# Kernel tuning notes

Hardware: AMD Instinct MI355X
Metric: run time of the kernel (lower is better)

## Reference

```python
import jax, jax.numpy as jnp
import numpy as np

EPS = 1e-10
TEMP = 1.0


def setup_inputs() -> dict:
    key = jax.random.key(0)
    ks = jax.random.split(key, 8)
    num_nodes, embed_dim, hidden_dim, num_edges = 50000, 128, 64, 600000
    node_embed = jax.random.normal(ks[0], (num_nodes, embed_dim), dtype=jnp.float32)
    edge_index = jax.random.randint(ks[1], (2, num_edges), 0, num_nodes, dtype=jnp.int64)
    u1 = jax.random.uniform(ks[2], (num_edges,), dtype=jnp.float32)
    u2 = jax.random.uniform(ks[3], (num_edges,), dtype=jnp.float32)
    # Linear weights (kaiming-ish scale)
    W1 = jax.random.normal(ks[4], (2 * embed_dim, hidden_dim), dtype=jnp.float32) * (1.0 / np.sqrt(2 * embed_dim))
    b1 = jnp.zeros((hidden_dim,), dtype=jnp.float32)
    W2 = jax.random.normal(ks[5], (hidden_dim, 1), dtype=jnp.float32) * (1.0 / np.sqrt(hidden_dim))
    b2 = jnp.zeros((1,), dtype=jnp.float32)
    return {"node_embed": node_embed, "edge_index": edge_index, "u1": u1, "u2": u2,
            "W1": W1, "b1": b1, "W2": W2, "b2": b2}


def reference(node_embed, edge_index, u1, u2, W1, b1, W2, b2):
    row, col = edge_index[0], edge_index[1]
    # gather + concat: [num_edges, 2*embed_dim]
    edge_feat = jnp.concatenate([node_embed[row], node_embed[col]], axis=1)
    # small MLP (dropout is identity in eval)
    h = jax.nn.relu(edge_feat @ W1 + b1)
    edge_logits = (h @ W2 + b2).squeeze(-1)  # [num_edges]
    # Gumbel-sigmoid (soft)
    g1 = -jnp.log(-jnp.log(jnp.clip(u1, EPS, 1.0 - EPS)))
    g2 = -jnp.log(-jnp.log(jnp.clip(u2, EPS, 1.0 - EPS)))
    edge_probs = jax.nn.sigmoid((edge_logits + g1 - g2) / TEMP)
    return edge_probs
```

## Files before the change

### kernel.cpp

```cpp
#include <hip/hip_runtime.h>
#include <stdint.h>

typedef float  floatx4 __attribute__((ext_vector_type(4)));
typedef short  short8  __attribute__((ext_vector_type(8)));
typedef float  f4v     __attribute__((ext_vector_type(4)));
typedef unsigned int uint32;

#define GS_EPS 1e-10f

__device__ __forceinline__ unsigned short f2bf(float x) {
  uint32 u = __float_as_uint(x);
  u += 0x7FFFu + ((u >> 16) & 1u);
  return (unsigned short)(u >> 16);
}

__device__ __forceinline__ float i8tof(uint32 w, int j) {
  int b = (int)(w << (24 - 8 * j)) >> 24;
  return (float)b;
}

__device__ __forceinline__ uint32 pack4_i8(floatx4 a, float inv) {
  uint32 r = 0;
#pragma unroll
  for (int i = 0; i < 4; ++i) {
    float x = a[i] * inv;
    x = fminf(fmaxf(x, -127.f), 127.f);
    int v = (int)__builtin_rintf(x);
    r |= ((uint32)(v & 255)) << (8 * i);
  }
  return r;
}

__global__ void conv_w1cat_kernel(const float* __restrict__ W1,
                                  unsigned short* __restrict__ w1g) {
  int i = blockIdx.x * 256 + threadIdx.x;
  int chunk = i >> 7;
  int n = i & 127;
  const float* src = (n < 64) ? (W1 + n) : (W1 + 128 * 64 + (n - 64));
  uint32 d[4];
#pragma unroll
  for (int j = 0; j < 4; ++j) {
    int k0 = chunk * 8 + 2 * j;
    unsigned short lo = f2bf(src[(size_t)k0 * 64]);
    unsigned short hi = f2bf(src[(size_t)(k0 + 1) * 64]);
    d[j] = (uint32)lo | ((uint32)hi << 16);
  }
#pragma unroll
  for (int j = 0; j < 4; ++j) *(uint32*)&w1g[(size_t)i * 8 + 2 * j] = d[j];
}

__global__ __launch_bounds__(512, 4) void pcompute_kernel(
    const float* __restrict__ E, const unsigned short* __restrict__ w1g,
    const float* __restrict__ b1,
    uint8_t* __restrict__ P8top, uint8_t* __restrict__ P8bot,
    float* __restrict__ Sct, float* __restrict__ Scb, int num_nodes) {
  __shared__ __align__(16) unsigned short w1blk[16 * 128 * 8];

  const int tid = threadIdx.x;
  const int wave = tid >> 6;
  const int lane = tid & 63;
  const int q = lane >> 4;
  const int l16 = lane & 15;

#pragma unroll
  for (int it = 0; it < 4; ++it) {
    int idx = it * 512 + tid;
    short8 v = *(const short8*)(w1g + (size_t)idx * 8);
    *(short8*)&w1blk[(size_t)idx * 8] = v;
  }

  const int rowbase = blockIdx.x * 128 + wave * 16;
  int row = rowbase + l16;
  const bool ok = row < num_nodes;
  if (!ok) row = num_nodes - 1;

  short8 bfr[4];
#pragma unroll
  for (int kk = 0; kk < 4; ++kk) {
    const float* p = E + (size_t)row * 128 + kk * 32 + q * 8;
    f4v v0 = *(const f4v*)p;
    f4v v1 = *(const f4v*)(p + 4);
    short8 t;
    t[0] = (short)f2bf(v0[0]); t[1] = (short)f2bf(v0[1]);
    t[2] = (short)f2bf(v0[2]); t[3] = (short)f2bf(v0[3]);
    t[4] = (short)f2bf(v1[0]); t[5] = (short)f2bf(v1[1]);
    t[6] = (short)f2bf(v1[2]); t[7] = (short)f2bf(v1[3]);
    bfr[kk] = t;
  }
  __syncthreads();

  floatx4 acc[8];
#pragma unroll
  for (int t = 0; t < 8; ++t) {
    floatx4 z = {0.f, 0.f, 0.f, 0.f};
    acc[t] = z;
  }
#pragma unroll
  for (int kk = 0; kk < 4; ++kk) {
#pragma unroll
    for (int t = 0; t < 8; ++t) {
      short8 af = *(const short8*)&w1blk[(size_t)((kk * 4 + q) * 128 + t * 16 + l16) * 8];
      acc[t] = __builtin_amdgcn_mfma_f32_16x16x32_bf16(af, bfr[kk], acc[t], 0, 0, 0);
    }
  }

  float mtop = 0.f, mbot = 0.f;
#pragma unroll
  for (int t = 0; t < 8; ++t) {
    floatx4 a = acc[t];
    if (t < 4) {
      f4v bv = *(const f4v*)(b1 + t * 16 + q * 4);
      a[0] += bv[0]; a[1] += bv[1]; a[2] += bv[2]; a[3] += bv[3];
      acc[t] = a;
      mtop = fmaxf(mtop, fmaxf(fmaxf(fabsf(a[0]), fabsf(a[1])),
                               fmaxf(fabsf(a[2]), fabsf(a[3]))));
    } else {
      mbot = fmaxf(mbot, fmaxf(fmaxf(fabsf(a[0]), fabsf(a[1])),
                               fmaxf(fabsf(a[2]), fabsf(a[3]))));
    }
  }
  mtop = fmaxf(mtop, __shfl_xor(mtop, 16, 64));
  mtop = fmaxf(mtop, __shfl_xor(mtop, 32, 64));
  mbot = fmaxf(mbot, __shfl_xor(mbot, 16, 64));
  mbot = fmaxf(mbot, __shfl_xor(mbot, 32, 64));
  const float invt = 127.f / fmaxf(mtop, 1e-20f);
  const float invb = 127.f / fmaxf(mbot, 1e-20f);

  if (ok) {
    const int node = rowbase + l16;
#pragma unroll
    for (int t = 0; t < 4; ++t) {
      *(uint32*)(P8top + (size_t)node * 64 + t * 16 + q * 4) = pack4_i8(acc[t], invt);
      *(uint32*)(P8bot + (size_t)node * 64 + t * 16 + q * 4) = pack4_i8(acc[4 + t], invb);
    }
    if (q == 0) {
      Sct[node] = mtop * (1.f / 127.f);
      Scb[node] = mbot * (1.f / 127.f);
    }
  }
}

__global__ __launch_bounds__(256, 8) void edge_kernel(
    const uint8_t* __restrict__ P8top, const uint8_t* __restrict__ P8bot,
    const float* __restrict__ Sct, const float* __restrict__ Scb,
    const int* __restrict__ ei,
    const float* __restrict__ u1, const float* __restrict__ u2,
    const float* __restrict__ W2, const float* __restrict__ b2,
    float* __restrict__ out, int num_edges) {
  const int tid = threadIdx.x;
  const int wave = tid >> 6;
  const int lane = tid & 63;
  const int g = lane >> 3;
  const int h = lane & 7;
  const int wbase = blockIdx.x * 128 + wave * 32;

  f4v w0 = *(const f4v*)(W2 + h * 8);
  f4v w1v = *(const f4v*)(W2 + h * 8 + 4);
  const float bias2 = b2[0];

  int el = wbase + (lane & 31);
  if (el > num_edges - 1) el = num_edges - 1;
  unsigned long long oddmask = __ballot(ei[2 * el + 1] != 0);
  const bool idx64 = (oddmask == 0ULL);
  int eR, eC;
  if (idx64) {
    eR = ei[2 * el];
    eC = ei[2 * (num_edges + el)];
  } else {
    eR = ei[el];
    eC = ei[num_edges + el];
  }

  uint2 ar[4], ac[4];
  float srv[4], scv[4];
#pragma unroll
  for (int s = 0; s < 4; ++s) {
    int nr = __shfl(eR, s * 8 + g, 64);
    int nc = __shfl(eC, s * 8 + g, 64);
    ar[s] = *(const uint2*)(P8top + (size_t)nr * 64 + h * 8);
    ac[s] = *(const uint2*)(P8bot + (size_t)nc * 64 + h * 8);
    srv[s] = Sct[nr];
    scv[s] = Scb[nc];
  }

#pragma unroll
  for (int s = 0; s < 4; ++s) {
    float accv = 0.f;
    const float sr = srv[s], sc = scv[s];
#pragma unroll
    for (int j = 0; j < 4; ++j) {
      float hv = fmaxf(i8tof(ar[s].x, j) * sr + i8tof(ac[s].x, j) * sc, 0.f);
      accv = fmaf(hv, w0[j], accv);
    }
#pragma unroll
    for (int j = 0; j < 4; ++j) {
      float hv = fmaxf(i8tof(ar[s].y, j) * sr + i8tof(ac[s].y, j) * sc, 0.f);
      accv = fmaf(hv, w1v[j], accv);
    }
    accv += __shfl_xor(accv, 1, 64);
    accv += __shfl_xor(accv, 2, 64);
    accv += __shfl_xor(accv, 4, 64);
    if (h == 0) {
      int e = wbase + s * 8 + g;
      if (e < num_edges) {
        float a1 = fminf(fmaxf(u1[e], GS_EPS), 1.0f);
        float a2 = fminf(fmaxf(u2[e], GS_EPS), 1.0f);
        float g1 = -__logf(-__logf(a1));
        float g2 = -__logf(-__logf(a2));
        float x = accv + bias2 + g1 - g2;
        out[e] = 1.f / (1.f + __expf(-x));
      }
    }
  }
}

extern "C" void kernel_launch(void* const* d_in, const int* in_sizes, int n_in,
                              void* d_out, int out_size, void* d_ws, size_t ws_size,
                              hipStream_t stream) {
  const float* node_embed = (const float*)d_in[0];
  const int* ei = (const int*)d_in[1];
  const float* u1 = (const float*)d_in[2];
  const float* u2 = (const float*)d_in[3];
  const float* W1 = (const float*)d_in[4];
  const float* b1 = (const float*)d_in[5];
  const float* W2 = (const float*)d_in[6];
  const float* b2 = (const float*)d_in[7];
  float* out = (float*)d_out;

  const int num_edges = in_sizes[2];
  const int num_nodes = in_sizes[0] / 128;

  char* w = (char*)d_ws;
  uint8_t* P8top = (uint8_t*)w;                  w += ((size_t)num_nodes * 64 + 255) & ~(size_t)255;
  uint8_t* P8bot = (uint8_t*)w;                  w += ((size_t)num_nodes * 64 + 255) & ~(size_t)255;
  float*   Sct   = (float*)w;                    w += ((size_t)num_nodes * 4 + 255) & ~(size_t)255;
  float*   Scb   = (float*)w;                    w += ((size_t)num_nodes * 4 + 255) & ~(size_t)255;
  unsigned short* w1g = (unsigned short*)w;

  conv_w1cat_kernel<<<8, 256, 0, stream>>>(W1, w1g);
  const int pblocks = (num_nodes + 127) / 128;
  pcompute_kernel<<<pblocks, 512, 0, stream>>>(node_embed, w1g, b1,
                                               P8top, P8bot, Sct, Scb, num_nodes);
  const int eblocks = (num_edges + 127) / 128;
  edge_kernel<<<eblocks, 256, 0, stream>>>(P8top, P8bot, Sct, Scb,
                                           ei, u1, u2, W2, b2, out, num_edges);
}
```

Measured before the change: 116.0 us.

## Interleave int8 top/bottom projections per node and use per-block quant scales

Merges the separate top and bottom int8 projection buffers into one 128-byte row per node, and replaces the per-node scale arrays with one float2 scale per 128-node block, computed by a cross-wave max reduction through shared memory. The edge kernel then reads both halves from one buffer and looks up the scale by node>>7. This is meant to cut scattered scale loads from large arrays to a small cached table. In exchange it adds a block-level sync and coarser quantization, which may reduce accuracy for nodes whose activations are much smaller than the block maximum.

```diff
diff --git a/kernel.cpp b/kernel.cpp
--- a/kernel.cpp
+++ b/kernel.cpp
@@ -13,12 +13,10 @@
   u += 0x7FFFu + ((u >> 16) & 1u);
   return (unsigned short)(u >> 16);
 }
-
 __device__ __forceinline__ float i8tof(uint32 w, int j) {
   int b = (int)(w << (24 - 8 * j)) >> 24;
   return (float)b;
 }
-
 __device__ __forceinline__ uint32 pack4_i8(floatx4 a, float inv) {
   uint32 r = 0;
 #pragma unroll
@@ -51,10 +49,10 @@
 
 __global__ __launch_bounds__(512, 4) void pcompute_kernel(
     const float* __restrict__ E, const unsigned short* __restrict__ w1g,
-    const float* __restrict__ b1,
-    uint8_t* __restrict__ P8top, uint8_t* __restrict__ P8bot,
-    float* __restrict__ Sct, float* __restrict__ Scb, int num_nodes) {
+    const float* __restrict__ b1, uint8_t* __restrict__ P8,
+    float2* __restrict__ Sc, int num_nodes) {
   __shared__ __align__(16) unsigned short w1blk[16 * 128 * 8];
+  __shared__ float wmt[8], wmb[8];
 
   const int tid = threadIdx.x;
   const int wave = tid >> 6;
@@ -112,37 +110,43 @@
       f4v bv = *(const f4v*)(b1 + t * 16 + q * 4);
       a[0] += bv[0]; a[1] += bv[1]; a[2] += bv[2]; a[3] += bv[3];
       acc[t] = a;
-      mtop = fmaxf(mtop, fmaxf(fmaxf(fabsf(a[0]), fabsf(a[1])),
-                               fmaxf(fabsf(a[2]), fabsf(a[3]))));
-    } else {
-      mbot = fmaxf(mbot, fmaxf(fmaxf(fabsf(a[0]), fabsf(a[1])),
-                               fmaxf(fabsf(a[2]), fabsf(a[3]))));
-    }
-  }
-  mtop = fmaxf(mtop, __shfl_xor(mtop, 16, 64));
-  mtop = fmaxf(mtop, __shfl_xor(mtop, 32, 64));
-  mbot = fmaxf(mbot, __shfl_xor(mbot, 16, 64));
-  mbot = fmaxf(mbot, __shfl_xor(mbot, 32, 64));
-  const float invt = 127.f / fmaxf(mtop, 1e-20f);
-  const float invb = 127.f / fmaxf(mbot, 1e-20f);
+    }
+    float m = fmaxf(fmaxf(fabsf(a[0]), fabsf(a[1])), fmaxf(fabsf(a[2]), fabsf(a[3])));
+    if (t < 4) mtop = fmaxf(mtop, m); else mbot = fmaxf(mbot, m);
+  }
+#pragma unroll
+  for (int s = 1; s < 64; s <<= 1) {
+    mtop = fmaxf(mtop, __shfl_xor(mtop, s, 64));
+    mbot = fmaxf(mbot, __shfl_xor(mbot, s, 64));
+  }
+  if (lane == 0) {
+    wmt[wave] = mtop;
+    wmb[wave] = mbot;
+  }
+  __syncthreads();
+  float bt = wmt[0], bb = wmb[0];
+#pragma unroll
+  for (int i = 1; i < 8; ++i) {
+    bt = fmaxf(bt, wmt[i]);
+    bb = fmaxf(bb, wmb[i]);
+  }
+  const float invt = 127.f / fmaxf(bt, 1e-20f);
+  const float invb = 127.f / fmaxf(bb, 1e-20f);
 
   if (ok) {
     const int node = rowbase + l16;
 #pragma unroll
-    for (int t = 0; t < 4; ++t) {
-      *(uint32*)(P8top + (size_t)node * 64 + t * 16 + q * 4) = pack4_i8(acc[t], invt);
-      *(uint32*)(P8bot + (size_t)node * 64 + t * 16 + q * 4) = pack4_i8(acc[4 + t], invb);
-    }
-    if (q == 0) {
-      Sct[node] = mtop * (1.f / 127.f);
-      Scb[node] = mbot * (1.f / 127.f);
-    }
-  }
+    for (int t = 0; t < 8; ++t) {
+      *(uint32*)(P8 + (size_t)node * 128 + t * 16 + q * 4) =
+          pack4_i8(acc[t], (t < 4) ? invt : invb);
+    }
+  }
+  if (tid == 0)
+    Sc[blockIdx.x] = make_float2(bt * (1.f / 127.f), bb * (1.f / 127.f));
 }
 
 __global__ __launch_bounds__(256, 8) void edge_kernel(
-    const uint8_t* __restrict__ P8top, const uint8_t* __restrict__ P8bot,
-    const float* __restrict__ Sct, const float* __restrict__ Scb,
+    const uint8_t* __restrict__ P8, const float2* __restrict__ Sc,
     const int* __restrict__ ei,
     const float* __restrict__ u1, const float* __restrict__ u2,
     const float* __restrict__ W2, const float* __restrict__ b2,
@@ -177,24 +181,24 @@
   for (int s = 0; s < 4; ++s) {
     int nr = __shfl(eR, s * 8 + g, 64);
     int nc = __shfl(eC, s * 8 + g, 64);
-    ar[s] = *(const uint2*)(P8top + (size_t)nr * 64 + h * 8);
-    ac[s] = *(const uint2*)(P8bot + (size_t)nc * 64 + h * 8);
-    srv[s] = Sct[nr];
-    scv[s] = Scb[nc];
+    ar[s] = *(const uint2*)(P8 + (size_t)nr * 128 + h * 8);
+    ac[s] = *(const uint2*)(P8 + (size_t)nc * 128 + 64 + h * 8);
+    srv[s] = Sc[nr >> 7].x;
+    scv[s] = Sc[nc >> 7].y;
   }
 
 #pragma unroll
   for (int s = 0; s < 4; ++s) {
     float accv = 0.f;
-    const float sr = srv[s], sc = scv[s];
+    const float st = srv[s], sb = scv[s];
 #pragma unroll
     for (int j = 0; j < 4; ++j) {
-      float hv = fmaxf(i8tof(ar[s].x, j) * sr + i8tof(ac[s].x, j) * sc, 0.f);
+      float hv = fmaxf(i8tof(ar[s].x, j) * st + i8tof(ac[s].x, j) * sb, 0.f);
       accv = fmaf(hv, w0[j], accv);
     }
 #pragma unroll
     for (int j = 0; j < 4; ++j) {
-      float hv = fmaxf(i8tof(ar[s].y, j) * sr + i8tof(ac[s].y, j) * sc, 0.f);
+      float hv = fmaxf(i8tof(ar[s].y, j) * st + i8tof(ac[s].y, j) * sb, 0.f);
       accv = fmaf(hv, w1v[j], accv);
     }
     accv += __shfl_xor(accv, 1, 64);
@@ -229,19 +233,15 @@
 
   const int num_edges = in_sizes[2];
   const int num_nodes = in_sizes[0] / 128;
+  const int pblocks = (num_nodes + 127) / 128;
 
   char* w = (char*)d_ws;
-  uint8_t* P8top = (uint8_t*)w;                  w += ((size_t)num_nodes * 64 + 255) & ~(size_t)255;
-  uint8_t* P8bot = (uint8_t*)w;                  w += ((size_t)num_nodes * 64 + 255) & ~(size_t)255;
-  float*   Sct   = (float*)w;                    w += ((size_t)num_nodes * 4 + 255) & ~(size_t)255;
-  float*   Scb   = (float*)w;                    w += ((size_t)num_nodes * 4 + 255) & ~(size_t)255;
+  uint8_t* P8 = (uint8_t*)w;   w += ((size_t)num_nodes * 128 + 255) & ~(size_t)255;
+  float2* Sc = (float2*)w;     w += ((size_t)pblocks * sizeof(float2) + 255) & ~(size_t)255;
   unsigned short* w1g = (unsigned short*)w;
 
   conv_w1cat_kernel<<<8, 256, 0, stream>>>(W1, w1g);
-  const int pblocks = (num_nodes + 127) / 128;
-  pcompute_kernel<<<pblocks, 512, 0, stream>>>(node_embed, w1g, b1,
-                                               P8top, P8bot, Sct, Scb, num_nodes);
+  pcompute_kernel<<<pblocks, 512, 0, stream>>>(node_embed, w1g, b1, P8, Sc, num_nodes);
   const int eblocks = (num_edges + 127) / 128;
-  edge_kernel<<<eblocks, 256, 0, stream>>>(P8top, P8bot, Sct, Scb,
-                                           ei, u1, u2, W2, b2, out, num_edges);
-}
+  edge_kernel<<<eblocks, 256, 0, stream>>>(P8, Sc, ei, u1, u2, W2, b2, out, num_edges);
+}
```

New measurement: 115.9 us. Within noise of the previous version (-0.1%).
